# Kernel tuning notes

Hardware: AMD Instinct MI355X
Metric: run time of the kernel (lower is better)

The kernel has to match this reference:

```python
import jax, jax.numpy as jnp
import numpy as np

NUM_NODES = 1_000_000
FEAT_DIM = 128
BATCH = 100_000
K = 16  # num_sample


def setup_inputs() -> dict:
    key = jax.random.key(0)
    k1, k2, k3 = jax.random.split(key, 3)
    features = jax.random.normal(k1, (NUM_NODES, FEAT_DIM), dtype=jnp.float32)
    nodes = jax.random.randint(k2, (BATCH,), 0, NUM_NODES, dtype=jnp.int64 if jax.config.read('jax_enable_x64') else jnp.int32)
    neigh_idx = jax.random.randint(k3, (BATCH, K), 0, NUM_NODES, dtype=jnp.int64 if jax.config.read('jax_enable_x64') else jnp.int32)
    return {"features": features, "nodes": nodes, "neigh_idx": neigh_idx, "num_sample": K}


def reference(features, nodes, neigh_idx, num_sample):
    # node's own features: [B, D]
    node_feats = features[nodes]
    # sampled neighbor gather [B, K, D] then mean over K (== sparse mm with 1/K weights)
    neigh_mean = jnp.mean(features[neigh_idx], axis=1)
    return node_feats + neigh_mean
```

## Files before the change

### kernel.cpp

```cpp
#include <hip/hip_runtime.h>


typedef float f32x4 __attribute__((ext_vector_type(4)));
typedef int   i32x4 __attribute__((ext_vector_type(4)));

constexpr int FEAT_DIM = 128;
constexpr int FEAT_Q   = FEAT_DIM / 4;
constexpr int K        = 16;

__global__ __launch_bounds__(256) void mean_agg_kernel(
    const float*  __restrict__ features,
    const int*    __restrict__ nodes,
    const int*    __restrict__ neigh_idx,
    float*        __restrict__ out,
    int batch)
{
    const int t = blockIdx.x * blockDim.x + threadIdx.x;
    const int b = t >> 5;
    if (b >= batch) return;
    const int cq = t & 31;

    const i32x4* ni = reinterpret_cast<const i32x4*>(neigh_idx) + (size_t)b * (K / 4);
    const i32x4 i0 = ni[0];
    const i32x4 i1 = ni[1];
    const i32x4 i2 = ni[2];
    const i32x4 i3 = ni[3];
    const int   nd = nodes[b];

    const f32x4* f4 = reinterpret_cast<const f32x4*>(features);

    auto row = [&](int idx) -> f32x4 {
        return f4[(size_t)idx * FEAT_Q + cq];
    };

    const f32x4 nf = row(nd);
    const f32x4 a0  = row(i0.x), a1  = row(i0.y), a2  = row(i0.z), a3  = row(i0.w);
    const f32x4 a4  = row(i1.x), a5  = row(i1.y), a6  = row(i1.z), a7  = row(i1.w);
    const f32x4 a8  = row(i2.x), a9  = row(i2.y), a10 = row(i2.z), a11 = row(i2.w);
    const f32x4 a12 = row(i3.x), a13 = row(i3.y), a14 = row(i3.z), a15 = row(i3.w);

    const f32x4 s =
        (((a0 + a1) + (a2 + a3)) + ((a4 + a5) + (a6 + a7))) +
        (((a8 + a9) + (a10 + a11)) + ((a12 + a13) + (a14 + a15)));

    constexpr float inv_k = 1.0f / (float)K;
    const f32x4 r = nf + s * inv_k;

    f32x4* op = reinterpret_cast<f32x4*>(out) + (size_t)b * FEAT_Q + cq;
    __builtin_nontemporal_store(r, op);
}

extern "C" void kernel_launch(void* const* d_in, const int* in_sizes, int n_in,
                              void* d_out, int out_size, void* d_ws, size_t ws_size,
                              hipStream_t stream) {
    const float* features  = (const float*)d_in[0];
    const int*   nodes     = (const int*)d_in[1];
    const int*   neigh_idx = (const int*)d_in[2];
    float* out = (float*)d_out;

    const int batch = in_sizes[1];
    const int total_threads = batch * 32;
    const int block = 256;
    const int grid  = (total_threads + block - 1) / block;

    mean_agg_kernel<<<grid, block, 0, stream>>>(features, nodes, neigh_idx, out, batch);
}
```

Measured before the change: 691.9 us.

## Map one wavefront per batch row with float2 lanes and scalar index loads

Each batch row is now handled by a full 64-lane wavefront using float2 loads instead of 32 threads with float4 loads. The row index is made wave-uniform via readfirstlane, so the neighbor indices can be fetched with scalar loads instead of per-lane vector loads. Launch bounds request higher occupancy. This doubles the thread count and uses narrower memory transactions per lane, trading vector width for more memory-level parallelism and less VGPR pressure.

```diff
diff --git a/kernel.cpp b/kernel.cpp
--- a/kernel.cpp
+++ b/kernel.cpp
@@ -1,14 +1,13 @@
 #include <hip/hip_runtime.h>
 
 
-typedef float f32x4 __attribute__((ext_vector_type(4)));
-typedef int   i32x4 __attribute__((ext_vector_type(4)));
+typedef float f32x2 __attribute__((ext_vector_type(2)));
 
 constexpr int FEAT_DIM = 128;
-constexpr int FEAT_Q   = FEAT_DIM / 4;
+constexpr int FEAT_H   = FEAT_DIM / 2;
 constexpr int K        = 16;
 
-__global__ __launch_bounds__(256) void mean_agg_kernel(
+__global__ __launch_bounds__(256, 8) void mean_agg_kernel(
     const float*  __restrict__ features,
     const int*    __restrict__ nodes,
     const int*    __restrict__ neigh_idx,
@@ -16,37 +15,38 @@
     int batch)
 {
     const int t = blockIdx.x * blockDim.x + threadIdx.x;
-    const int b = t >> 5;
+    int b = t >> 6;
     if (b >= batch) return;
-    const int cq = t & 31;
+    b = __builtin_amdgcn_readfirstlane(b);
+    const int lane = t & 63;
 
-    const i32x4* ni = reinterpret_cast<const i32x4*>(neigh_idx) + (size_t)b * (K / 4);
-    const i32x4 i0 = ni[0];
-    const i32x4 i1 = ni[1];
-    const i32x4 i2 = ni[2];
-    const i32x4 i3 = ni[3];
-    const int   nd = nodes[b];
+    const int* ni = neigh_idx + (size_t)b * K;
+    int idx0  = ni[0],  idx1  = ni[1],  idx2  = ni[2],  idx3  = ni[3];
+    int idx4  = ni[4],  idx5  = ni[5],  idx6  = ni[6],  idx7  = ni[7];
+    int idx8  = ni[8],  idx9  = ni[9],  idx10 = ni[10], idx11 = ni[11];
+    int idx12 = ni[12], idx13 = ni[13], idx14 = ni[14], idx15 = ni[15];
+    const int nd = nodes[b];
 
-    const f32x4* f4 = reinterpret_cast<const f32x4*>(features);
+    const f32x2* f2 = reinterpret_cast<const f32x2*>(features);
 
-    auto row = [&](int idx) -> f32x4 {
-        return f4[(size_t)idx * FEAT_Q + cq];
+    auto row = [&](int idx) -> f32x2 {
+        return f2[(size_t)idx * FEAT_H + lane];
     };
 
-    const f32x4 nf = row(nd);
-    const f32x4 a0  = row(i0.x), a1  = row(i0.y), a2  = row(i0.z), a3  = row(i0.w);
-    const f32x4 a4  = row(i1.x), a5  = row(i1.y), a6  = row(i1.z), a7  = row(i1.w);
-    const f32x4 a8  = row(i2.x), a9  = row(i2.y), a10 = row(i2.z), a11 = row(i2.w);
-    const f32x4 a12 = row(i3.x), a13 = row(i3.y), a14 = row(i3.z), a15 = row(i3.w);
+    const f32x2 nf  = row(nd);
+    const f32x2 a0  = row(idx0),  a1  = row(idx1),  a2  = row(idx2),  a3  = row(idx3);
+    const f32x2 a4  = row(idx4),  a5  = row(idx5),  a6  = row(idx6),  a7  = row(idx7);
+    const f32x2 a8  = row(idx8),  a9  = row(idx9),  a10 = row(idx10), a11 = row(idx11);
+    const f32x2 a12 = row(idx12), a13 = row(idx13), a14 = row(idx14), a15 = row(idx15);
 
-    const f32x4 s =
+    const f32x2 s =
         (((a0 + a1) + (a2 + a3)) + ((a4 + a5) + (a6 + a7))) +
         (((a8 + a9) + (a10 + a11)) + ((a12 + a13) + (a14 + a15)));
 
     constexpr float inv_k = 1.0f / (float)K;
-    const f32x4 r = nf + s * inv_k;
+    const f32x2 r = nf + s * inv_k;
 
-    f32x4* op = reinterpret_cast<f32x4*>(out) + (size_t)b * FEAT_Q + cq;
+    f32x2* op = reinterpret_cast<f32x2*>(out) + (size_t)b * FEAT_H + lane;
     __builtin_nontemporal_store(r, op);
 }
 
@@ -59,9 +59,9 @@
     float* out = (float*)d_out;
 
     const int batch = in_sizes[1];
-    const int total_threads = batch * 32;
+    const long long total_threads = (long long)batch * 64;
     const int block = 256;
-    const int grid  = (total_threads + block - 1) / block;
+    const int grid  = (int)((total_threads + block - 1) / block);
 
     mean_agg_kernel<<<grid, block, 0, stream>>>(features, nodes, neigh_idx, out, batch);
 }
```

Measured after the change: 693.9 us. About the same (+0.3%).
